# Optimization experiments

Hardware: AMD Instinct MI355X
Metric: run time of the kernel (lower is better)

The kernel has to match this reference:

```python
import jax, jax.numpy as jnp
import numpy as np

N = 50000      # nodes
E = 800000     # edges (avg degree 16)
IN = 512       # input features
OUT = 32       # per-head hidden features
H = 8          # heads (layer 1)
C = 16         # classes (layer 2, 1 head)
NEG_SLOPE = 0.2


def setup_inputs() -> dict:
    key = jax.random.key(0)
    ks = jax.random.split(key, 8)
    x = jax.random.normal(ks[0], (N, IN), jnp.float32)
    edge_index = jax.random.randint(ks[1], (2, E), 0, N, jnp.int32)
    # layer 1 params: W1 [IN, H*OUT], attention vectors a1_src/a1_dst [H, OUT]
    W1 = jax.random.normal(ks[2], (IN, H * OUT), jnp.float32) * (1.0 / np.sqrt(IN))
    a1_src = jax.random.normal(ks[3], (H, OUT), jnp.float32) * (1.0 / np.sqrt(OUT))
    a1_dst = jax.random.normal(ks[4], (H, OUT), jnp.float32) * (1.0 / np.sqrt(OUT))
    # layer 2 params: single head, W2 [H*OUT, C], a2_src/a2_dst [1, C]
    W2 = jax.random.normal(ks[5], (H * OUT, C), jnp.float32) * (1.0 / np.sqrt(H * OUT))
    a2_src = jax.random.normal(ks[6], (1, C), jnp.float32) * (1.0 / np.sqrt(C))
    a2_dst = jax.random.normal(ks[7], (1, C), jnp.float32) * (1.0 / np.sqrt(C))
    return {"x": x, "W1": W1, "a1_src": a1_src, "a1_dst": a1_dst,
            "W2": W2, "a2_src": a2_src, "a2_dst": a2_dst,
            "edge_index": edge_index}


def gat_layer(x, edge_index, W, a_src, a_dst, concat):
    """Standard GAT layer: e_ij = LeakyReLU(a_src.Wh_i + a_dst.Wh_j),
    softmax over incoming edges of each target node, scatter-aggregate."""
    n = x.shape[0]
    h_heads, f = a_src.shape
    h = (x @ W).reshape(n, h_heads, f)                      # [N, H, F]
    src, dst = edge_index[0], edge_index[1]
    es = jnp.einsum('nhf,hf->nh', h, a_src)                 # [N, H] per-node src scores
    ed = jnp.einsum('nhf,hf->nh', h, a_dst)                 # [N, H]
    e = jax.nn.leaky_relu(es[src] + ed[dst], NEG_SLOPE)     # [E, H] per-edge logits
    # segment softmax over edges grouped by dst node
    m = jax.ops.segment_max(e, dst, num_segments=n)         # [N, H]
    m = jnp.where(jnp.isfinite(m), m, 0.0)                  # empty segments -> -inf
    p = jnp.exp(e - m[dst])                                 # [E, H]
    s = jax.ops.segment_sum(p, dst, num_segments=n)         # [N, H]
    denom = s[dst]
    alpha = p / jnp.where(denom > 0, denom, 1.0)            # [E, H]
    msg = h[src] * alpha[:, :, None]                        # [E, H, F]
    out = jax.ops.segment_sum(msg, dst, num_segments=n)     # [N, H, F]
    if concat:
        return out.reshape(n, h_heads * f)
    return out.mean(axis=1)


def reference(x, W1, a1_src, a1_dst, W2, a2_src, a2_dst, edge_index):
    # dropout is identity in eval mode
    h = gat_layer(x, edge_index, W1, a1_src, a1_dst, concat=True)   # [N, H*OUT]
    h = jax.nn.elu(h)
    h = gat_layer(h, edge_index, W2, a2_src, a2_dst, concat=False)  # [N, C]
    return jax.nn.log_softmax(h, axis=1)
```

## Files before the change

### kernel.cpp

```cpp
#include <hip/hip_runtime.h>

#define NN 50000
#define EE 800000
#define KIN 512
#define HF 256
#define NH 8
#define FOUT 32
#define NC 16
#define NEG 0.2f
#define NB_SCAN 196

typedef unsigned short u16;
typedef __attribute__((ext_vector_type(8))) short shortx8;
typedef __attribute__((ext_vector_type(4))) float floatx4;
typedef __attribute__((ext_vector_type(8))) unsigned short ushortx8;
typedef __attribute__((ext_vector_type(4))) unsigned uintx4;

__device__ __forceinline__ float lrelu(float x) { return x > 0.f ? x : NEG * x; }

__device__ __forceinline__ u16 f2bf(float f) {
    unsigned u = __float_as_uint(f);
    return (u16)((u + 0x7FFFu + ((u >> 16) & 1u)) >> 16);
}
__device__ __forceinline__ float bf2f(u16 v) {
    return __uint_as_float((unsigned)v << 16);
}
__device__ __forceinline__ unsigned pk2bf(float a, float b) {
    unsigned ua = __float_as_uint(a), ub = __float_as_uint(b);
    return ((ua + 0x8000u) >> 16) | ((ub + 0x8000u) & 0xffff0000u);
}

__device__ __forceinline__ void gll16(const void* g, void* l) {
    __builtin_amdgcn_global_load_lds((const __attribute__((address_space(1))) void*)g,
                                     (__attribute__((address_space(3))) void*)l, 16, 0, 0);
}

__global__ void count_deg(const int* __restrict__ dst, int* __restrict__ deg) {
    int e = blockIdx.x * 256 + threadIdx.x;
    if (e < EE) atomicAdd(&deg[dst[e]], 1);
}

__global__ __launch_bounds__(256) void scan_a(const int* __restrict__ deg, int* __restrict__ bsum) {
    __shared__ int sm[256];
    int t = threadIdx.x;
    int i = blockIdx.x * 256 + t;
    sm[t] = (i < NN) ? deg[i] : 0;
    __syncthreads();
    for (int o = 128; o; o >>= 1) { if (t < o) sm[t] += sm[t + o]; __syncthreads(); }
    if (t == 0) bsum[blockIdx.x] = sm[0];
}

__global__ __launch_bounds__(256) void scan_b(const int* __restrict__ bsum, int* __restrict__ boff) {
    __shared__ int sm[256];
    int t = threadIdx.x;
    sm[t] = (t < NB_SCAN) ? bsum[t] : 0;
    __syncthreads();
    for (int d = 1; d < 256; d <<= 1) {
        int v = (t >= d) ? sm[t - d] : 0;
        __syncthreads();
        sm[t] += v;
        __syncthreads();
    }
    if (t < NB_SCAN) boff[t] = (t == 0) ? 0 : sm[t - 1];
}

__global__ __launch_bounds__(256) void scan_c(const int* __restrict__ deg, const int* __restrict__ boff,
                                              int* __restrict__ off) {
    __shared__ int sm[256];
    int t = threadIdx.x;
    int i = blockIdx.x * 256 + t;
    int d = (i < NN) ? deg[i] : 0;
    sm[t] = d;
    __syncthreads();
    for (int dd = 1; dd < 256; dd <<= 1) {
        int v = (t >= dd) ? sm[t - dd] : 0;
        __syncthreads();
        sm[t] += v;
        __syncthreads();
    }
    if (i < NN) off[i] = boff[blockIdx.x] + sm[t] - d;
    if (i == 0) off[NN] = EE;
}

__global__ void fill_csr(const int* __restrict__ src, const int* __restrict__ dst,
                         const int* __restrict__ off, int* __restrict__ cursor,
                         int* __restrict__ csr_src) {
    int e = blockIdx.x * 256 + threadIdx.x;
    if (e < EE) {
        int d = dst[e];
        int pos = atomicAdd(&cursor[d], 1);
        csr_src[off[d] + pos] = src[e];
    }
}

__global__ __launch_bounds__(256) void convert_w(const float* __restrict__ W1, const float* __restrict__ W2,
                                                 u16* __restrict__ w1t, u16* __restrict__ w2t) {
    int e = blockIdx.x * 256 + threadIdx.x;
    if (e < KIN * HF) {
        int k = e >> 8, n = e & 255;
        w1t[n * KIN + k] = f2bf(W1[e]);
    } else {
        int e2 = e - KIN * HF;
        if (e2 < HF * NC) {
            int k = e2 >> 4, c = e2 & 15;
            w2t[c * HF + k] = f2bf(W2[e2]);
        }
    }
}

__global__ __launch_bounds__(256, 2) void gemm1_mfma(const float* __restrict__ x,
                                                     const u16* __restrict__ w1t,
                                                     u16* __restrict__ h1b) {
    __shared__ __align__(16) float As[128 * 32];
    __shared__ __align__(16) u16 Bs[256 * 32];
    int t = threadIdx.x;
    int lane = t & 63, wave = t >> 6;
    int wm = wave >> 1, wn = wave & 1;
    int lm = lane & 15, quad = lane >> 4;
    int bm = blockIdx.x * 128;

    floatx4 acc[4][8];
#pragma unroll
    for (int i = 0; i < 4; i++)
#pragma unroll
        for (int j = 0; j < 8; j++) acc[i][j] = (floatx4){0.f, 0.f, 0.f, 0.f};

    int arow_l = wave * 32 + (lane >> 3);
    int akoff = (lane & 7) * 4;
    const float* aptr[4];
#pragma unroll
    for (int i = 0; i < 4; i++) {
        int ar = bm + arow_l + i * 8;
        if (ar > NN - 1) ar = NN - 1;
        aptr[i] = x + (size_t)ar * KIN + akoff;
    }
    float* alds[4];
#pragma unroll
    for (int i = 0; i < 4; i++) alds[i] = As + (wave * 32 + i * 8) * 32;

    int brow_l = wave * 64 + (lane >> 2);
    int bkoff = (lane & 3) * 8;
    const u16* bptr[4];
#pragma unroll
    for (int i = 0; i < 4; i++) bptr[i] = w1t + (size_t)(brow_l + i * 16) * KIN + bkoff;
    u16* blds[4];
#pragma unroll
    for (int i = 0; i < 4; i++) blds[i] = Bs + (wave * 64 + i * 16) * 32;

    int offA[4], offB[8];
#pragma unroll
    for (int i = 0; i < 4; i++) offA[i] = (wm * 64 + i * 16 + lm) * 32 + quad * 8;
#pragma unroll
    for (int j = 0; j < 8; j++) offB[j] = (wn * 128 + j * 16 + lm) * 32 + quad * 8;

    for (int kk = 0; kk < KIN; kk += 32) {
#pragma unroll
        for (int i = 0; i < 4; i++) gll16(aptr[i] + kk, alds[i]);
#pragma unroll
        for (int i = 0; i < 4; i++) gll16(bptr[i] + kk, blds[i]);
        __syncthreads();
        shortx8 af[4], bf[8];
#pragma unroll
        for (int i = 0; i < 4; i++) {
            const float4* ap = (const float4*)&As[offA[i]];
            float4 lo = ap[0], hi = ap[1];
            union { uintx4 u; shortx8 s; } cv;
            cv.u[0] = pk2bf(lo.x, lo.y);
            cv.u[1] = pk2bf(lo.z, lo.w);
            cv.u[2] = pk2bf(hi.x, hi.y);
            cv.u[3] = pk2bf(hi.z, hi.w);
            af[i] = cv.s;
        }
#pragma unroll
        for (int j = 0; j < 8; j++) bf[j] = *(const shortx8*)&Bs[offB[j]];
#pragma unroll
        for (int i = 0; i < 4; i++)
#pragma unroll
            for (int j = 0; j < 8; j++)
                acc[i][j] = __builtin_amdgcn_mfma_f32_16x16x32_bf16(af[i], bf[j], acc[i][j], 0, 0, 0);
        __syncthreads();
    }

#pragma unroll
    for (int i = 0; i < 4; i++) {
        int row = bm + wm * 64 + i * 16 + quad * 4;
#pragma unroll
        for (int j = 0; j < 8; j++) {
            int col = wn * 128 + j * 16 + lm;
#pragma unroll
            for (int r = 0; r < 4; r++) {
                if (row + r < NN) h1b[(size_t)(row + r) * HF + col] = f2bf(acc[i][j][r]);
            }
        }
    }
}

__global__ __launch_bounds__(256) void scores1(const u16* __restrict__ h1b, const float* __restrict__ a_src,
                                               const float* __restrict__ a_dst,
                                               float* __restrict__ es, float* __restrict__ ed) {
    __shared__ float as_s[HF], ad_s[HF];
    int t = threadIdx.x;
    as_s[t] = a_src[t];
    ad_s[t] = a_dst[t];
    __syncthreads();
    int nl = t >> 5;
    int L = t & 31;
    int n = blockIdx.x * 8 + nl;
    ushortx8 hv = *(const ushortx8*)(h1b + (size_t)n * HF + L * 8);
    float ps = 0.f, pd = 0.f;
#pragma unroll
    for (int i = 0; i < 8; i++) {
        float v = bf2f(hv[i]);
        ps += v * as_s[L * 8 + i];
        pd += v * ad_s[L * 8 + i];
    }
    ps += __shfl_down(ps, 2, 4); ps += __shfl_down(ps, 1, 4);
    pd += __shfl_down(pd, 2, 4); pd += __shfl_down(pd, 1, 4);
    if ((L & 3) == 0) {
        int h = L >> 2;
        es[n * NH + h] = ps;
        ed[n * NH + h] = pd;
    }
}

__global__ __launch_bounds__(256) void agg1(const u16* __restrict__ h1b, const float* __restrict__ es,
                                            const float* __restrict__ ed, const int* __restrict__ off,
                                            const int* __restrict__ csr_src, u16* __restrict__ out1b) {
    int wave = threadIdx.x >> 6;
    int lane = threadIdx.x & 63;
    int n = blockIdx.x * 4 + wave;
    int fh = lane & 31;
    int ep = lane >> 5;
    int head = fh >> 2;
    int beg = off[n];
    int deg = off[n + 1] - beg;
    float edh = ed[n * NH + head];
    const u16* hbase = h1b + fh * 8;
    float acc[8] = {0.f, 0.f, 0.f, 0.f, 0.f, 0.f, 0.f, 0.f};
    float s_part = 0.f;
    for (int base = 0; base < deg; base += 16) {
        int nch = deg - base; if (nch > 16) nch = 16;
        int sv = (lane < nch) ? csr_src[beg + base + lane] : 0;
#pragma unroll
        for (int e = 0; e < 8; e++) {
            int ee = 2 * e + ep;
            int s = __shfl(sv, ee, 64);
            if (ee < nch) {
                float lg = es[s * NH + head] + edh;
                float p = __expf(lg > 0.f ? lg : NEG * lg);
                ushortx8 hv = *(const ushortx8*)(hbase + (size_t)s * HF);
                s_part += p;
#pragma unroll
                for (int i = 0; i < 8; i++) acc[i] += p * bf2f(hv[i]);
            }
        }
    }
#pragma unroll
    for (int i = 0; i < 8; i++) acc[i] += __shfl_down(acc[i], 32, 64);
    s_part += __shfl_down(s_part, 32, 64);
    if (lane < 32) {
        float inv = s_part > 0.f ? 1.0f / s_part : 0.f;
        union { uintx4 u; ushortx8 v; } ob;
#pragma unroll
        for (int i = 0; i < 4; i++) {
            float v0 = acc[2 * i] * inv, v1 = acc[2 * i + 1] * inv;
            v0 = v0 > 0.f ? v0 : (__expf(v0) - 1.0f);
            v1 = v1 > 0.f ? v1 : (__expf(v1) - 1.0f);
            ob.u[i] = (unsigned)f2bf(v0) | ((unsigned)f2bf(v1) << 16);
        }
        *(ushortx8*)(out1b + (size_t)n * HF + fh * 8) = ob.v;
    }
}

__global__ __launch_bounds__(64) void gemm2_mfma(const u16* __restrict__ out1b, const u16* __restrict__ w2t,
                                                 const float* __restrict__ a2s, const float* __restrict__ a2d,
                                                 float* __restrict__ h2, float* __restrict__ es2,
                                                 float* __restrict__ ed2) {
    int lane = threadIdx.x;
    int lm = lane & 15, quad = lane >> 4;
    int nb = blockIdx.x * 16;
    floatx4 acc = (floatx4){0.f, 0.f, 0.f, 0.f};
    const u16* arow = out1b + (size_t)(nb + lm) * HF + quad * 8;
    const u16* brow = w2t + lm * HF + quad * 8;
#pragma unroll
    for (int kk = 0; kk < HF; kk += 32) {
        shortx8 af = *(const shortx8*)(arow + kk);
        shortx8 bf = *(const shortx8*)(brow + kk);
        acc = __builtin_amdgcn_mfma_f32_16x16x32_bf16(af, bf, acc, 0, 0, 0);
    }
    float a2sc = a2s[lm], a2dc = a2d[lm];
#pragma unroll
    for (int r = 0; r < 4; r++) {
        int n = nb + quad * 4 + r;
        float v = acc[r];
        h2[n * NC + lm] = v;
        float ps = v * a2sc, pd = v * a2dc;
#pragma unroll
        for (int o = 8; o; o >>= 1) {
            ps += __shfl_down(ps, o, 16);
            pd += __shfl_down(pd, o, 16);
        }
        if (lm == 0) { es2[n] = ps; ed2[n] = pd; }
    }
}

__global__ __launch_bounds__(256) void agg2(const float* __restrict__ h2, const float* __restrict__ es2,
                                            const float* __restrict__ ed2, const int* __restrict__ off,
                                            const int* __restrict__ csr_src, float* __restrict__ out) {
    int t = threadIdx.x;
    int nid = blockIdx.x * 16 + (t >> 4);
    int c = t & 15;
    int beg = off[nid];
    int deg = off[nid + 1] - beg;
    float edn = ed2[nid];
    float s = 0.f, acc = 0.f;
    for (int base = 0; base < deg; base += 16) {
        int nch = deg - base; if (nch > 16) nch = 16;
        int sv = 0;
        if (c < nch) sv = csr_src[beg + base + c];
        int sva[16];
#pragma unroll
        for (int e = 0; e < 16; e++) sva[e] = __shfl(sv, e, 16);
        float hva[16];
#pragma unroll
        for (int e = 0; e < 16; e++) hva[e] = h2[sva[e] * NC + c];
        float p = 0.f;
        if (c < nch) p = __expf(lrelu(es2[sv] + edn));
        s += p;
        float pa[16];
#pragma unroll
        for (int e = 0; e < 16; e++) pa[e] = __shfl(p, e, 16);
#pragma unroll
        for (int e = 0; e < 16; e++) acc += pa[e] * hva[e];
    }
#pragma unroll
    for (int o = 8; o; o >>= 1) s += __shfl_down(s, o, 16);
    s = __shfl(s, 0, 16);
    float v = (s > 0.f) ? acc / s : 0.f;
    float m2 = v;
#pragma unroll
    for (int o = 8; o; o >>= 1) m2 = fmaxf(m2, __shfl_down(m2, o, 16));
    m2 = __shfl(m2, 0, 16);
    float se = __expf(v - m2);
#pragma unroll
    for (int o = 8; o; o >>= 1) se += __shfl_down(se, o, 16);
    se = __shfl(se, 0, 16);
    out[nid * NC + c] = v - m2 - __logf(se);
}

extern "C" void kernel_launch(void* const* d_in, const int* in_sizes, int n_in,
                              void* d_out, int out_size, void* d_ws, size_t ws_size,
                              hipStream_t stream) {
    const float* x   = (const float*)d_in[0];
    const float* W1  = (const float*)d_in[1];
    const float* a1s = (const float*)d_in[2];
    const float* a1d = (const float*)d_in[3];
    const float* W2  = (const float*)d_in[4];
    const float* a2s = (const float*)d_in[5];
    const float* a2d = (const float*)d_in[6];
    const int*   ei  = (const int*)d_in[7];
    const int* srcv = ei;
    const int* dstv = ei + EE;
    float* out = (float*)d_out;

    u16* h1b    = (u16*)d_ws;
    u16* out1b  = h1b + (size_t)NN * HF;
    float* es1  = (float*)(out1b + (size_t)NN * HF);
    float* ed1  = es1 + (size_t)NN * NH;
    float* h2   = ed1 + (size_t)NN * NH;
    float* es2v = h2 + (size_t)NN * NC;
    float* ed2v = es2v + NN;
    int* deg    = (int*)(ed2v + NN);
    int* cursor = deg + NN;
    int* offs   = cursor + NN;
    int* csr    = offs + NN + 1;
    int* bsum   = csr + EE;
    int* boff   = bsum + 256;
    u16* w1t    = (u16*)(boff + 256);
    u16* w2t    = w1t + (size_t)HF * KIN;

    hipMemsetAsync(deg, 0, 2 * NN * sizeof(int), stream);
    count_deg<<<(EE + 255) / 256, 256, 0, stream>>>(dstv, deg);
    scan_a<<<NB_SCAN, 256, 0, stream>>>(deg, bsum);
    scan_b<<<1, 256, 0, stream>>>(bsum, boff);
    scan_c<<<NB_SCAN, 256, 0, stream>>>(deg, boff, offs);
    fill_csr<<<(EE + 255) / 256, 256, 0, stream>>>(srcv, dstv, offs, cursor, csr);
    convert_w<<<(KIN * HF + HF * NC + 255) / 256, 256, 0, stream>>>(W1, W2, w1t, w2t);
    gemm1_mfma<<<(NN + 127) / 128, 256, 0, stream>>>(x, w1t, h1b);
    scores1<<<NN / 8, 256, 0, stream>>>(h1b, a1s, a1d, es1, ed1);
    agg1<<<NN / 4, 256, 0, stream>>>(h1b, es1, ed1, offs, csr, out1b);
    gemm2_mfma<<<NN / 16, 64, 0, stream>>>(out1b, w2t, a2s, a2d, h2, es2v, ed2v);
    agg2<<<NN / 16, 256, 0, stream>>>(h2, es2v, ed2v, offs, csr, out);
}
```

Baseline: 360.7 us.

## Fuse weight conversion, scan pass, and score epilogue; store layer-2 features as bf16

Merges the weight conversion into the degree-count kernel and drops the single-block scan_b by having each scan_c block reduce the preceding block sums itself. It computes the layer-1 attention scores in the GEMM epilogue from the fp32 accumulators, which removes the separate scores1 kernel and its re-read of h1. It also stores h2 in bf16 to halve the gather traffic in agg2. Together these cut three kernel launches and some memory traffic, at the cost of extra shuffles in the GEMM epilogue and a small precision loss in layer 2.

```diff
diff --git a/kernel.cpp b/kernel.cpp
--- a/kernel.cpp
+++ b/kernel.cpp
@@ -35,9 +35,19 @@
                                      (__attribute__((address_space(3))) void*)l, 16, 0, 0);
 }
 
-__global__ void count_deg(const int* __restrict__ dst, int* __restrict__ deg) {
+__global__ void count_deg_convw(const int* __restrict__ dst, int* __restrict__ deg,
+                                const float* __restrict__ W1, const float* __restrict__ W2,
+                                u16* __restrict__ w1t, u16* __restrict__ w2t) {
     int e = blockIdx.x * 256 + threadIdx.x;
     if (e < EE) atomicAdd(&deg[dst[e]], 1);
+    if (e < KIN * HF) {
+        int k = e >> 8, n = e & 255;
+        w1t[n * KIN + k] = f2bf(W1[e]);
+    } else if (e < KIN * HF + HF * NC) {
+        int e2 = e - KIN * HF;
+        int k = e2 >> 4, c = e2 & 15;
+        w2t[c * HF + k] = f2bf(W2[e2]);
+    }
 }
 
 __global__ __launch_bounds__(256) void scan_a(const int* __restrict__ deg, int* __restrict__ bsum) {
@@ -50,24 +60,16 @@
     if (t == 0) bsum[blockIdx.x] = sm[0];
 }
 
-__global__ __launch_bounds__(256) void scan_b(const int* __restrict__ bsum, int* __restrict__ boff) {
-    __shared__ int sm[256];
-    int t = threadIdx.x;
-    sm[t] = (t < NB_SCAN) ? bsum[t] : 0;
-    __syncthreads();
-    for (int d = 1; d < 256; d <<= 1) {
-        int v = (t >= d) ? sm[t - d] : 0;
-        __syncthreads();
-        sm[t] += v;
-        __syncthreads();
-    }
-    if (t < NB_SCAN) boff[t] = (t == 0) ? 0 : sm[t - 1];
-}
-
-__global__ __launch_bounds__(256) void scan_c(const int* __restrict__ deg, const int* __restrict__ boff,
+__global__ __launch_bounds__(256) void scan_c(const int* __restrict__ deg, const int* __restrict__ bsum,
                                               int* __restrict__ off) {
     __shared__ int sm[256];
+    __shared__ int pre[256];
     int t = threadIdx.x;
+    pre[t] = (t < blockIdx.x && t < NB_SCAN) ? bsum[t] : 0;
+    __syncthreads();
+    for (int o = 128; o; o >>= 1) { if (t < o) pre[t] += pre[t + o]; __syncthreads(); }
+    int bofs = pre[0];
+    __syncthreads();
     int i = blockIdx.x * 256 + t;
     int d = (i < NN) ? deg[i] : 0;
     sm[t] = d;
@@ -78,7 +80,7 @@
         sm[t] += v;
         __syncthreads();
     }
-    if (i < NN) off[i] = boff[blockIdx.x] + sm[t] - d;
+    if (i < NN) off[i] = bofs + sm[t] - d;
     if (i == 0) off[NN] = EE;
 }
 
@@ -93,24 +95,13 @@
     }
 }
 
-__global__ __launch_bounds__(256) void convert_w(const float* __restrict__ W1, const float* __restrict__ W2,
-                                                 u16* __restrict__ w1t, u16* __restrict__ w2t) {
-    int e = blockIdx.x * 256 + threadIdx.x;
-    if (e < KIN * HF) {
-        int k = e >> 8, n = e & 255;
-        w1t[n * KIN + k] = f2bf(W1[e]);
-    } else {
-        int e2 = e - KIN * HF;
-        if (e2 < HF * NC) {
-            int k = e2 >> 4, c = e2 & 15;
-            w2t[c * HF + k] = f2bf(W2[e2]);
-        }
-    }
-}
-
 __global__ __launch_bounds__(256, 2) void gemm1_mfma(const float* __restrict__ x,
                                                      const u16* __restrict__ w1t,
-                                                     u16* __restrict__ h1b) {
+                                                     u16* __restrict__ h1b,
+                                                     const float* __restrict__ a1s,
+                                                     const float* __restrict__ a1d,
+                                                     float* __restrict__ es1,
+                                                     float* __restrict__ ed1) {
     __shared__ __align__(16) float As[128 * 32];
     __shared__ __align__(16) u16 Bs[256 * 32];
     int t = threadIdx.x;
@@ -193,33 +184,35 @@
             }
         }
     }
-}
-
-__global__ __launch_bounds__(256) void scores1(const u16* __restrict__ h1b, const float* __restrict__ a_src,
-                                               const float* __restrict__ a_dst,
-                                               float* __restrict__ es, float* __restrict__ ed) {
-    __shared__ float as_s[HF], ad_s[HF];
-    int t = threadIdx.x;
-    as_s[t] = a_src[t];
-    ad_s[t] = a_dst[t];
-    __syncthreads();
-    int nl = t >> 5;
-    int L = t & 31;
-    int n = blockIdx.x * 8 + nl;
-    ushortx8 hv = *(const ushortx8*)(h1b + (size_t)n * HF + L * 8);
-    float ps = 0.f, pd = 0.f;
-#pragma unroll
-    for (int i = 0; i < 8; i++) {
-        float v = bf2f(hv[i]);
-        ps += v * as_s[L * 8 + i];
-        pd += v * ad_s[L * 8 + i];
-    }
-    ps += __shfl_down(ps, 2, 4); ps += __shfl_down(ps, 1, 4);
-    pd += __shfl_down(pd, 2, 4); pd += __shfl_down(pd, 1, 4);
-    if ((L & 3) == 0) {
-        int h = L >> 2;
-        es[n * NH + h] = ps;
-        ed[n * NH + h] = pd;
+
+    float as_v[8], ad_v[8];
+#pragma unroll
+    for (int j = 0; j < 8; j++) {
+        int col = wn * 128 + j * 16 + lm;
+        as_v[j] = a1s[col];
+        ad_v[j] = a1d[col];
+    }
+#pragma unroll
+    for (int i = 0; i < 4; i++) {
+#pragma unroll
+        for (int r = 0; r < 4; r++) {
+            int row = bm + wm * 64 + i * 16 + quad * 4 + r;
+#pragma unroll
+            for (int hp = 0; hp < 4; hp++) {
+                float e_s = acc[i][2 * hp][r] * as_v[2 * hp] + acc[i][2 * hp + 1][r] * as_v[2 * hp + 1];
+                float e_d = acc[i][2 * hp][r] * ad_v[2 * hp] + acc[i][2 * hp + 1][r] * ad_v[2 * hp + 1];
+#pragma unroll
+                for (int o = 8; o; o >>= 1) {
+                    e_s += __shfl_down(e_s, o, 16);
+                    e_d += __shfl_down(e_d, o, 16);
+                }
+                if (lm == 0 && row < NN) {
+                    int h = wn * 4 + hp;
+                    es1[row * NH + h] = e_s;
+                    ed1[row * NH + h] = e_d;
+                }
+            }
+        }
     }
 }
 
@@ -274,7 +267,7 @@
 
 __global__ __launch_bounds__(64) void gemm2_mfma(const u16* __restrict__ out1b, const u16* __restrict__ w2t,
                                                  const float* __restrict__ a2s, const float* __restrict__ a2d,
-                                                 float* __restrict__ h2, float* __restrict__ es2,
+                                                 u16* __restrict__ h2b, float* __restrict__ es2,
                                                  float* __restrict__ ed2) {
     int lane = threadIdx.x;
     int lm = lane & 15, quad = lane >> 4;
@@ -293,7 +286,7 @@
     for (int r = 0; r < 4; r++) {
         int n = nb + quad * 4 + r;
         float v = acc[r];
-        h2[n * NC + lm] = v;
+        h2b[n * NC + lm] = f2bf(v);
         float ps = v * a2sc, pd = v * a2dc;
 #pragma unroll
         for (int o = 8; o; o >>= 1) {
@@ -304,7 +297,7 @@
     }
 }
 
-__global__ __launch_bounds__(256) void agg2(const float* __restrict__ h2, const float* __restrict__ es2,
+__global__ __launch_bounds__(256) void agg2(const u16* __restrict__ h2b, const float* __restrict__ es2,
                                             const float* __restrict__ ed2, const int* __restrict__ off,
                                             const int* __restrict__ csr_src, float* __restrict__ out) {
     int t = threadIdx.x;
@@ -323,7 +316,7 @@
         for (int e = 0; e < 16; e++) sva[e] = __shfl(sv, e, 16);
         float hva[16];
 #pragma unroll
-        for (int e = 0; e < 16; e++) hva[e] = h2[sva[e] * NC + c];
+        for (int e = 0; e < 16; e++) hva[e] = bf2f(h2b[sva[e] * NC + c]);
         float p = 0.f;
         if (c < nch) p = __expf(lrelu(es2[sv] + edn));
         s += p;
@@ -367,28 +360,24 @@
     u16* out1b  = h1b + (size_t)NN * HF;
     float* es1  = (float*)(out1b + (size_t)NN * HF);
     float* ed1  = es1 + (size_t)NN * NH;
-    float* h2   = ed1 + (size_t)NN * NH;
-    float* es2v = h2 + (size_t)NN * NC;
+    u16* h2b    = (u16*)(ed1 + (size_t)NN * NH);
+    float* es2v = (float*)(h2b + (size_t)NN * NC);
     float* ed2v = es2v + NN;
     int* deg    = (int*)(ed2v + NN);
     int* cursor = deg + NN;
     int* offs   = cursor + NN;
     int* csr    = offs + NN + 1;
     int* bsum   = csr + EE;
-    int* boff   = bsum + 256;
-    u16* w1t    = (u16*)(boff + 256);
+    u16* w1t    = (u16*)(bsum + 256);
     u16* w2t    = w1t + (size_t)HF * KIN;
 
     hipMemsetAsync(deg, 0, 2 * NN * sizeof(int), stream);
-    count_deg<<<(EE + 255) / 256, 256, 0, stream>>>(dstv, deg);
+    count_deg_convw<<<(EE + 255) / 256, 256, 0, stream>>>(dstv, deg, W1, W2, w1t, w2t);
     scan_a<<<NB_SCAN, 256, 0, stream>>>(deg, bsum);
-    scan_b<<<1, 256, 0, stream>>>(bsum, boff);
-    scan_c<<<NB_SCAN, 256, 0, stream>>>(deg, boff, offs);
+    scan_c<<<NB_SCAN, 256, 0, stream>>>(deg, bsum, offs);
     fill_csr<<<(EE + 255) / 256, 256, 0, stream>>>(srcv, dstv, offs, cursor, csr);
-    convert_w<<<(KIN * HF + HF * NC + 255) / 256, 256, 0, stream>>>(W1, W2, w1t, w2t);
-    gemm1_mfma<<<(NN + 127) / 128, 256, 0, stream>>>(x, w1t, h1b);
-    scores1<<<NN / 8, 256, 0, stream>>>(h1b, a1s, a1d, es1, ed1);
+    gemm1_mfma<<<(NN + 127) / 128, 256, 0, stream>>>(x, w1t, h1b, a1s, a1d, es1, ed1);
     agg1<<<NN / 4, 256, 0, stream>>>(h1b, es1, ed1, offs, csr, out1b);
-    gemm2_mfma<<<NN / 16, 64, 0, stream>>>(out1b, w2t, a2s, a2d, h2, es2v, ed2v);
-    agg2<<<NN / 16, 256, 0, stream>>>(h2, es2v, ed2v, offs, csr, out);
-}
+    gemm2_mfma<<<NN / 16, 64, 0, stream>>>(out1b, w2t, a2s, a2d, h2b, es2v, ed2v);
+    agg2<<<NN / 16, 256, 0, stream>>>(h2b, es2v, ed2v, offs, csr, out);
+}
```

Measured after the change: 360.2 us. Within noise of the previous version (-0.1%).
